# Kernel tuning notes

Measured on AMD Instinct MI355X. Metric: run time of the kernel, lower is better.

## Reference

```python
import jax, jax.numpy as jnp
import numpy as np

EMB = 2048
HEADS = 8
HEAD_DIM = EMB // HEADS  # 256

def setup_inputs() -> dict:
    key = jax.random.key(0)
    ks = jax.random.split(key, 4)
    b, n = 2, 2048
    x = jax.random.normal(ks[0], (b, n, EMB), dtype=jnp.float32)
    # Linear weights stored as [in, out] (y = x @ W + b)
    w_qkv = jax.random.normal(ks[1], (EMB, 3 * EMB), dtype=jnp.float32) * (EMB ** -0.5)
    b_qkv = jnp.zeros((3 * EMB,), dtype=jnp.float32)
    w_proj = jax.random.normal(ks[2], (EMB, EMB), dtype=jnp.float32) * (EMB ** -0.5)
    b_proj = jnp.zeros((EMB,), dtype=jnp.float32)
    return {"x": x, "w_qkv": w_qkv, "b_qkv": b_qkv, "w_proj": w_proj, "b_proj": b_proj}

def reference(x, w_qkv, b_qkv, w_proj, b_proj):
    b, n, _ = x.shape
    qkv = x @ w_qkv + b_qkv                                   # [b, n, 3*emb]
    # rearrange 'b n (h d qkv) -> qkv b h n d': qkv index is innermost
    qkv = qkv.reshape(b, n, HEADS, HEAD_DIM, 3)
    qkv = jnp.transpose(qkv, (4, 0, 2, 1, 3))                 # [3, b, h, n, d]
    q, k, v = qkv[0], qkv[1], qkv[2]
    energy = jnp.einsum('bhqd,bhkd->bhqk', q, k)              # [b, h, n, n]
    scaling = EMB ** 0.5
    # NOTE: faithful to source — softmax on UNSCALED logits, divide after.
    att = jax.nn.softmax(energy, axis=-1) / scaling
    out = jnp.einsum('bhal,bhlv->bhav', att, v)               # [b, h, n, d]
    out = jnp.transpose(out, (0, 2, 1, 3)).reshape(b, n, EMB)  # b n (h d)
    return out @ w_proj + b_proj
```

## Files before the change

kernel.cpp:

```cpp
#include <hip/hip_runtime.h>
#include <cstdint>
#include <cstddef>


typedef __bf16 bf16x8 __attribute__((ext_vector_type(8)));
typedef __bf16 bf16x2 __attribute__((ext_vector_type(2)));
typedef float f32x4 __attribute__((ext_vector_type(4)));

#define SCALE_INV 0.022097086912079608f

#define GLDS16(gp, lp)                                                        \
  __builtin_amdgcn_global_load_lds(                                           \
      (const __attribute__((address_space(1))) void*)(gp),                    \
      (__attribute__((address_space(3))) void*)(lp), 16, 0, 0)

__device__ inline void split8(const float4 v0, const float4 v1, bf16x8& hi,
                              bf16x8& lo) {
  float a[8] = {v0.x, v0.y, v0.z, v0.w, v1.x, v1.y, v1.z, v1.w};
  bf16x8 h, l;
#pragma unroll
  for (int i = 0; i < 8; i++) {
    __bf16 hh = (__bf16)a[i];
    h[i] = hh;
    l[i] = (__bf16)(a[i] - (float)hh);
  }
  hi = h;
  lo = l;
}

__global__ __launch_bounds__(256) void transpose_cvt_k(
    const float* __restrict__ in, __bf16* __restrict__ out, int R, int C) {
  __shared__ float tile[32][33];
  const int tx = threadIdx.x & 31;
  const int ty = threadIdx.x >> 5;
  const int c0 = blockIdx.x * 32;
  const int r0 = blockIdx.y * 32;
#pragma unroll
  for (int i = 0; i < 32; i += 8)
    tile[ty + i][tx] = in[(size_t)(r0 + ty + i) * C + (c0 + tx)];
  __syncthreads();
#pragma unroll
  for (int i = 0; i < 32; i += 8)
    out[(size_t)(c0 + ty + i) * R + (r0 + tx)] = (__bf16)tile[tx][ty + i];
}

__global__ __launch_bounds__(256) void transpose_w_split_k(
    const float* __restrict__ in, __bf16* __restrict__ wh,
    __bf16* __restrict__ wl1, __bf16* __restrict__ wl2) {
  __shared__ float tile[64][65];
  const int tid = threadIdx.x;
  const int c0 = blockIdx.x * 64;
  const int r0 = blockIdx.y * 64;
  const int cx = tid & 15, ry = tid >> 4;
#pragma unroll
  for (int p = 0; p < 4; p++) {
    const float4 v =
        *(const float4*)&in[(size_t)(r0 + p * 16 + ry) * 6144 + c0 + cx * 4];
    tile[p * 16 + ry][cx * 4 + 0] = v.x;
    tile[p * 16 + ry][cx * 4 + 1] = v.y;
    tile[p * 16 + ry][cx * 4 + 2] = v.z;
    tile[p * 16 + ry][cx * 4 + 3] = v.w;
  }
  __syncthreads();
  const int r2 = tid & 31;
  const int cy = tid >> 5;
  __bf16* wlb = (c0 < 2048) ? wl1 + (size_t)c0 * 2048
                            : wl2 + (size_t)(c0 - 2048) * 2048;
#pragma unroll
  for (int p = 0; p < 8; p++) {
    const int cl = cy + p * 8;
    const float t0 = tile[2 * r2][cl];
    const float t1 = tile[2 * r2 + 1][cl];
    const __bf16 h0 = (__bf16)t0, h1 = (__bf16)t1;
    bf16x2 hv = {h0, h1};
    bf16x2 lv = {(__bf16)(t0 - (float)h0), (__bf16)(t1 - (float)h1)};
    *(bf16x2*)&wh[(size_t)(c0 + cl) * 2048 + r0 + 2 * r2] = hv;
    *(bf16x2*)&wlb[(size_t)cl * 2048 + r0 + 2 * r2] = lv;
  }
}

__global__ __launch_bounds__(256) void gemm_qkv_split_k(
    const float* __restrict__ X, const __bf16* __restrict__ Wh,
    const __bf16* __restrict__ Wl1, const __bf16* __restrict__ Wl2,
    const float* __restrict__ bias, __bf16* __restrict__ qh_,
    __bf16* __restrict__ ql_, __bf16* __restrict__ kh_,
    __bf16* __restrict__ kl_, __bf16* __restrict__ vT) {
  __shared__ __bf16 Ah[128 * 40], Al[128 * 40];
  __shared__ __attribute__((aligned(16))) __bf16 BhL[2 * 4096];
  __shared__ __attribute__((aligned(16))) __bf16 BlL[2 * 4096];
  const int tid = threadIdx.x, lane = tid & 63, wave = tid >> 6;
  const int l16 = lane & 15, quad = lane >> 4;
  const int wm = (wave >> 1) * 64, wn = (wave & 1) * 64;
  const int bid = blockIdx.y * 48 + blockIdx.x;
  const int nb2 = (bid & 7) * 192 + (bid >> 3);
  const int m0 = (nb2 / 48) * 128, n0 = (nb2 % 48) * 128;
  const int r0 = tid >> 2, kc0 = (tid & 3) * 8;

  f32x4 zero4 = {0.f, 0.f, 0.f, 0.f};
  f32x4 acc[4][4];
#pragma unroll
  for (int i = 0; i < 4; i++)
#pragma unroll
    for (int j = 0; j < 4; j++) acc[i][j] = zero4;

  const float* Arow0 = X + (size_t)(m0 + r0) * 2048 + kc0;
  const float* Arow1 = Arow0 + (size_t)64 * 2048;
  const __bf16* BhP = Wh + (size_t)n0 * 2048;
  const __bf16* BlP = (n0 < 2048) ? Wl1 + (size_t)n0 * 2048
                                  : Wl2 + (size_t)(n0 - 2048) * 2048;

  const int rowl = lane >> 2, gq = lane & 3;
  const int sg = gq ^ (rowl & 3);
  size_t bSrc[2];
  int bDst[2];
#pragma unroll
  for (int i = 0; i < 2; i++) {
    const int row = wave * 32 + i * 16 + rowl;
    bSrc[i] = (size_t)row * 2048 + sg * 8;
    bDst[i] = (wave * 32 + i * 16) * 32;
  }
  const int bro = (wn + l16) * 32 + ((quad ^ (l16 & 3)) << 3);

  GLDS16(BhP + bSrc[0], &BhL[bDst[0]]);
  GLDS16(BhP + bSrc[1], &BhL[bDst[1]]);
  GLDS16(BlP + bSrc[0], &BlL[bDst[0]]);
  GLDS16(BlP + bSrc[1], &BlL[bDst[1]]);
  float4 a00 = *(const float4*)(Arow0);
  float4 a01 = *(const float4*)(Arow0 + 4);
  float4 a10 = *(const float4*)(Arow1);
  float4 a11 = *(const float4*)(Arow1 + 4);
  bf16x8 ah0, al0, ah1, al1;
  split8(a00, a01, ah0, al0);
  split8(a10, a11, ah1, al1);
  *(bf16x8*)&Ah[r0 * 40 + kc0] = ah0;
  *(bf16x8*)&Al[r0 * 40 + kc0] = al0;
  *(bf16x8*)&Ah[(r0 + 64) * 40 + kc0] = ah1;
  *(bf16x8*)&Al[(r0 + 64) * 40 + kc0] = al1;

  for (int k0 = 0; k0 < 2048; k0 += 32) {
    const int cur = (k0 >> 5) & 1;
    const int cb = cur * 4096;
    __syncthreads();
    const int nxt = k0 + 32;
    if (nxt < 2048) {
      const int nb = (cur ^ 1) * 4096;
      GLDS16(BhP + bSrc[0] + nxt, &BhL[nb + bDst[0]]);
      GLDS16(BhP + bSrc[1] + nxt, &BhL[nb + bDst[1]]);
      GLDS16(BlP + bSrc[0] + nxt, &BlL[nb + bDst[0]]);
      GLDS16(BlP + bSrc[1] + nxt, &BlL[nb + bDst[1]]);
      a00 = *(const float4*)(Arow0 + nxt);
      a01 = *(const float4*)(Arow0 + nxt + 4);
      a10 = *(const float4*)(Arow1 + nxt);
      a11 = *(const float4*)(Arow1 + nxt + 4);
    }
    bf16x8 fah[4], fal[4], fbh[4], fbl[4];
#pragma unroll
    for (int i = 0; i < 4; i++) {
      fah[i] = *(const bf16x8*)&Ah[(wm + i * 16 + l16) * 40 + quad * 8];
      fal[i] = *(const bf16x8*)&Al[(wm + i * 16 + l16) * 40 + quad * 8];
    }
#pragma unroll
    for (int j = 0; j < 4; j++) {
      fbh[j] = *(const bf16x8*)&BhL[cb + bro + j * 512];
      fbl[j] = *(const bf16x8*)&BlL[cb + bro + j * 512];
    }
#pragma unroll
    for (int i = 0; i < 4; i++)
#pragma unroll
      for (int j = 0; j < 4; j++) {
        acc[i][j] = __builtin_amdgcn_mfma_f32_16x16x32_bf16(fah[i], fbh[j],
                                                            acc[i][j], 0, 0, 0);
        acc[i][j] = __builtin_amdgcn_mfma_f32_16x16x32_bf16(fah[i], fbl[j],
                                                            acc[i][j], 0, 0, 0);
        acc[i][j] = __builtin_amdgcn_mfma_f32_16x16x32_bf16(fal[i], fbh[j],
                                                            acc[i][j], 0, 0, 0);
      }
    if (nxt < 2048) {
      split8(a00, a01, ah0, al0);
      split8(a10, a11, ah1, al1);
      __syncthreads();
      *(bf16x8*)&Ah[r0 * 40 + kc0] = ah0;
      *(bf16x8*)&Al[r0 * 40 + kc0] = al0;
      *(bf16x8*)&Ah[(r0 + 64) * 40 + kc0] = ah1;
      *(bf16x8*)&Al[(r0 + 64) * 40 + kc0] = al1;
    }
  }

#pragma unroll
  for (int i = 0; i < 4; i++) {
#pragma unroll
    for (int j = 0; j < 4; j++) {
      const int col = n0 + wn + j * 16 + l16;
      const float bv = bias[col];
      const int h = col / 768;
      const int rr = col - h * 768;
      const int d = rr / 3;
      const int c = rr - d * 3;
#pragma unroll
      for (int r = 0; r < 4; r++) {
        const int row = m0 + wm + i * 16 + quad * 4 + r;
        const float v = acc[i][j][r] + bv;
        const int b = row >> 11;
        const int nn = row & 2047;
        const int bh = b * 8 + h;
        const size_t idx = ((size_t)bh * 2048 + nn) * 256 + d;
        if (c == 0) {
          __bf16 hi = (__bf16)v;
          qh_[idx] = hi;
          ql_[idx] = (__bf16)(v - (float)hi);
        } else if (c == 1) {
          __bf16 hi = (__bf16)v;
          kh_[idx] = hi;
          kl_[idx] = (__bf16)(v - (float)hi);
        } else {
          vT[((size_t)bh * 256 + d) * 2048 + nn] = (__bf16)v;
        }
      }
    }
  }
}

__global__ __launch_bounds__(256, 2) void attn_fwd_k(
    const __bf16* __restrict__ Qh,
    const __bf16* __restrict__ Ql,
    const __bf16* __restrict__ Kh,
    const __bf16* __restrict__ Kl,
    const __bf16* __restrict__ Vt,
    __bf16* __restrict__ out) {
  __shared__ __attribute__((aligned(16))) __bf16 KhL[64 * 256];
  __shared__ __attribute__((aligned(16))) __bf16 KlL[64 * 256];
  __shared__ __attribute__((aligned(16))) __bf16 Plds[4][16 * 72];

  const int qblk = blockIdx.x;
  const int bh = blockIdx.y;
  const int bb = bh >> 3, hh = bh & 7;
  const int tid = threadIdx.x, lane = tid & 63, wave = tid >> 6;
  const int l16 = lane & 15, quad = lane >> 4;

  const size_t hqk = (size_t)bh * 2048 * 256;
  const __bf16* qhp = Qh + hqk;
  const __bf16* qlp = Ql + hqk;
  const __bf16* khp = Kh + hqk;
  const __bf16* klp = Kl + hqk;
  const __bf16* vp = Vt + (size_t)bh * 256 * 2048;

  const int qrow = qblk * 64 + wave * 16;

  bf16x8 qhf[8], qlf[8];
#pragma unroll
  for (int t = 0; t < 8; t++) {
    const size_t off = (size_t)(qrow + l16) * 256 + t * 32 + quad * 8;
    qhf[t] = *(const bf16x8*)&qhp[off];
    qlf[t] = *(const bf16x8*)&qlp[off];
  }

  f32x4 zero4 = {0.f, 0.f, 0.f, 0.f};
  f32x4 o[16];
#pragma unroll
  for (int dt = 0; dt < 16; dt++) o[dt] = zero4;
  float mrow[4], lrow[4];
#pragma unroll
  for (int r = 0; r < 4; r++) {
    mrow[r] = -3.0e38f;
    lrow[r] = 0.f;
  }

  int koff[8];
#pragma unroll
  for (int i = 0; i < 8; i++) {
    const int r = wave * 16 + i * 2 + (lane >> 5);
    const int cb = ((lane & 31) << 4) ^ ((r & 7) << 4);
    koff[i] = r * 256 + (cb >> 1);
  }
  const int ldsb = wave * 4096;

#pragma unroll
  for (int i = 0; i < 8; i++) {
    GLDS16(khp + koff[i], &KhL[ldsb + i * 512]);
    GLDS16(klp + koff[i], &KlL[ldsb + i * 512]);
  }

  for (int kv0 = 0; kv0 < 2048; kv0 += 64) {
    __syncthreads();

    f32x4 s[4];
#pragma unroll
    for (int j = 0; j < 4; j++) s[j] = zero4;
    __builtin_amdgcn_s_setprio(1);
#pragma unroll
    for (int j = 0; j < 4; j++) {
      const int row = j * 16 + l16;
      const int swz = (row & 7) << 3;
      const int rb = row * 256;
#pragma unroll
      for (int t = 0; t < 8; t++) {
        const int off = rb + ((t * 32 + quad * 8) ^ swz);
        bf16x8 khf = *(const bf16x8*)&KhL[off];
        bf16x8 klf = *(const bf16x8*)&KlL[off];
        s[j] =
            __builtin_amdgcn_mfma_f32_16x16x32_bf16(qhf[t], khf, s[j], 0, 0, 0);
        s[j] =
            __builtin_amdgcn_mfma_f32_16x16x32_bf16(qhf[t], klf, s[j], 0, 0, 0);
        s[j] =
            __builtin_amdgcn_mfma_f32_16x16x32_bf16(qlf[t], khf, s[j], 0, 0, 0);
      }
    }
    __builtin_amdgcn_s_setprio(0);
    __syncthreads();

    if (kv0 + 64 < 2048) {
      const int kvn = (kv0 + 64) * 256;
#pragma unroll
      for (int i = 0; i < 8; i++) {
        GLDS16(khp + kvn + koff[i], &KhL[ldsb + i * 512]);
        GLDS16(klp + kvn + koff[i], &KlL[ldsb + i * 512]);
      }
    }

    float mnew[4], alpha[4], psum[4];
#pragma unroll
    for (int r = 0; r < 4; r++) {
      float mx = fmaxf(fmaxf(s[0][r], s[1][r]), fmaxf(s[2][r], s[3][r]));
#pragma unroll
      for (int off = 1; off < 16; off <<= 1)
        mx = fmaxf(mx, __shfl_xor(mx, off, 16));
      mnew[r] = fmaxf(mrow[r], mx);
      alpha[r] = __expf(mrow[r] - mnew[r]);
      psum[r] = 0.f;
    }
#pragma unroll
    for (int j = 0; j < 4; j++)
#pragma unroll
      for (int r = 0; r < 4; r++) {
        float p = __expf(s[j][r] - mnew[r]);
        s[j][r] = p;
        psum[r] += p;
      }
#pragma unroll
    for (int r = 0; r < 4; r++) {
#pragma unroll
      for (int off = 1; off < 16; off <<= 1)
        psum[r] += __shfl_xor(psum[r], off, 16);
      lrow[r] = lrow[r] * alpha[r] + psum[r];
      mrow[r] = mnew[r];
    }
#pragma unroll
    for (int dt = 0; dt < 16; dt++) {
      o[dt][0] *= alpha[0];
      o[dt][1] *= alpha[1];
      o[dt][2] *= alpha[2];
      o[dt][3] *= alpha[3];
    }
#pragma unroll
    for (int j = 0; j < 4; j++)
#pragma unroll
      for (int r = 0; r < 4; r++)
        Plds[wave][(quad * 4 + r) * 72 + j * 16 + l16] = (__bf16)s[j][r];
    bf16x8 pa0 = *(const bf16x8*)&Plds[wave][l16 * 72 + quad * 8];
    bf16x8 pa1 = *(const bf16x8*)&Plds[wave][l16 * 72 + 32 + quad * 8];

    __builtin_amdgcn_s_setprio(1);
#pragma unroll
    for (int dt = 0; dt < 16; dt++) {
      const __bf16* vr = vp + (size_t)(dt * 16 + l16) * 2048 + kv0 + quad * 8;
      bf16x8 vf0 = *(const bf16x8*)vr;
      bf16x8 vf1 = *(const bf16x8*)(vr + 32);
      o[dt] = __builtin_amdgcn_mfma_f32_16x16x32_bf16(pa0, vf0, o[dt], 0, 0, 0);
      o[dt] = __builtin_amdgcn_mfma_f32_16x16x32_bf16(pa1, vf1, o[dt], 0, 0, 0);
    }
    __builtin_amdgcn_s_setprio(0);
  }

#pragma unroll
  for (int r = 0; r < 4; r++) {
    const float inv = SCALE_INV / lrow[r];
    const int n = qrow + quad * 4 + r;
    const size_t base = ((size_t)bb * 2048 + n) * 2048 + hh * 256;
#pragma unroll
    for (int dt = 0; dt < 16; dt++)
      out[base + dt * 16 + l16] = (__bf16)(o[dt][r] * inv);
  }
}

__global__ __launch_bounds__(256) void gemm_bt_k(
    const __bf16* __restrict__ A, const __bf16* __restrict__ Bt,
    const float* __restrict__ bias, int M, int Ncols, int K,
    float* __restrict__ outF) {
  __shared__ __bf16 As[128 * 40];
  __shared__ __bf16 Bs[128 * 40];
  const int tid = threadIdx.x, lane = tid & 63, wave = tid >> 6;
  const int l16 = lane & 15, quad = lane >> 4;
  const int wm = (wave >> 1) * 64, wn = (wave & 1) * 64;
  const int m0 = blockIdx.y * 128, n0 = blockIdx.x * 128;
  const int r0 = tid >> 2, kc0 = (tid & 3) * 8;

  f32x4 zero4 = {0.f, 0.f, 0.f, 0.f};
  f32x4 acc[4][4];
#pragma unroll
  for (int i = 0; i < 4; i++)
#pragma unroll
    for (int j = 0; j < 4; j++) acc[i][j] = zero4;

  const __bf16* Aptr = A + (size_t)(m0 + r0) * K + kc0;
  const __bf16* Bptr = Bt + (size_t)(n0 + r0) * K + kc0;
  const size_t rowstep = (size_t)64 * K;

  for (int k0 = 0; k0 < K; k0 += 32) {
    uint4 a0 = *(const uint4*)(Aptr + k0);
    uint4 a1 = *(const uint4*)(Aptr + rowstep + k0);
    uint4 b0 = *(const uint4*)(Bptr + k0);
    uint4 b1 = *(const uint4*)(Bptr + rowstep + k0);
    __syncthreads();
    *(uint4*)&As[r0 * 40 + kc0] = a0;
    *(uint4*)&As[(r0 + 64) * 40 + kc0] = a1;
    *(uint4*)&Bs[r0 * 40 + kc0] = b0;
    *(uint4*)&Bs[(r0 + 64) * 40 + kc0] = b1;
    __syncthreads();
    bf16x8 af[4], bfv[4];
#pragma unroll
    for (int i = 0; i < 4; i++)
      af[i] = *(const bf16x8*)&As[(wm + i * 16 + l16) * 40 + quad * 8];
#pragma unroll
    for (int j = 0; j < 4; j++)
      bfv[j] = *(const bf16x8*)&Bs[(wn + j * 16 + l16) * 40 + quad * 8];
#pragma unroll
    for (int i = 0; i < 4; i++)
#pragma unroll
      for (int j = 0; j < 4; j++)
        acc[i][j] = __builtin_amdgcn_mfma_f32_16x16x32_bf16(af[i], bfv[j],
                                                            acc[i][j], 0, 0, 0);
  }

#pragma unroll
  for (int i = 0; i < 4; i++)
#pragma unroll
    for (int j = 0; j < 4; j++) {
      const int col = n0 + wn + j * 16 + l16;
      const float bv = bias[col];
#pragma unroll
      for (int r = 0; r < 4; r++) {
        const int row = m0 + wm + i * 16 + quad * 4 + r;
        outF[(size_t)row * Ncols + col] = acc[i][j][r] + bv;
      }
    }
}

extern "C" void kernel_launch(void* const* d_in, const int* in_sizes, int n_in,
                              void* d_out, int out_size, void* d_ws,
                              size_t ws_size, hipStream_t stream) {
  const float* x = (const float*)d_in[0];
  const float* w_qkv = (const float*)d_in[1];
  const float* b_qkv = (const float*)d_in[2];
  const float* w_proj = (const float*)d_in[3];
  const float* b_proj = (const float*)d_in[4];
  float* out = (float*)d_out;

  const size_t HSZ = (size_t)16 * 2048 * 256;
  __bf16* qh = (__bf16*)d_ws;
  __bf16* ql = qh + HSZ;
  __bf16* kh = ql + HSZ;
  __bf16* kl = kh + HSZ;
  __bf16* vT = kl + HSZ;
  __bf16* attn = vT + HSZ;
  __bf16* wprojT = qh;

  __bf16* wh = (__bf16*)out;
  __bf16* wl1 = wh + (size_t)6144 * 2048;
  __bf16* wl2 = attn;

  transpose_w_split_k<<<dim3(96, 32), 256, 0, stream>>>(w_qkv, wh, wl1, wl2);
  gemm_qkv_split_k<<<dim3(48, 32), 256, 0, stream>>>(x, wh, wl1, wl2, b_qkv,
                                                     qh, ql, kh, kl, vT);
  attn_fwd_k<<<dim3(32, 16), 256, 0, stream>>>(qh, ql, kh, kl, vT, attn);
  transpose_cvt_k<<<dim3(64, 64), 256, 0, stream>>>(w_proj, wprojT, 2048, 2048);
  gemm_bt_k<<<dim3(16, 32), 256, 0, stream>>>(attn, wprojT, b_proj, 4096, 2048,
                                              2048, out);
}
```

Baseline: 973.5 us.

## Double-buffer A tile in QKV GEMM, drop mid-loop barrier, use linear block mapping

```diff
diff --git a/kernel.cpp b/kernel.cpp
--- a/kernel.cpp
+++ b/kernel.cpp
@@ -85,15 +85,13 @@
     const float* __restrict__ bias, __bf16* __restrict__ qh_,
     __bf16* __restrict__ ql_, __bf16* __restrict__ kh_,
     __bf16* __restrict__ kl_, __bf16* __restrict__ vT) {
-  __shared__ __bf16 Ah[128 * 40], Al[128 * 40];
-  __shared__ __attribute__((aligned(16))) __bf16 BhL[2 * 4096];
-  __shared__ __attribute__((aligned(16))) __bf16 BlL[2 * 4096];
+  __shared__ __bf16 Ah[2][128 * 40], Al[2][128 * 40];
+  __shared__ __attribute__((aligned(16))) __bf16 BhL[2][4096];
+  __shared__ __attribute__((aligned(16))) __bf16 BlL[2][4096];
   const int tid = threadIdx.x, lane = tid & 63, wave = tid >> 6;
   const int l16 = lane & 15, quad = lane >> 4;
   const int wm = (wave >> 1) * 64, wn = (wave & 1) * 64;
-  const int bid = blockIdx.y * 48 + blockIdx.x;
-  const int nb2 = (bid & 7) * 192 + (bid >> 3);
-  const int m0 = (nb2 / 48) * 128, n0 = (nb2 % 48) * 128;
+  const int m0 = blockIdx.y * 128, n0 = blockIdx.x * 128;
   const int r0 = tid >> 2, kc0 = (tid & 3) * 8;
 
   f32x4 zero4 = {0.f, 0.f, 0.f, 0.f};
@@ -121,48 +119,46 @@
   }
   const int bro = (wn + l16) * 32 + ((quad ^ (l16 & 3)) << 3);
 
-  GLDS16(BhP + bSrc[0], &BhL[bDst[0]]);
-  GLDS16(BhP + bSrc[1], &BhL[bDst[1]]);
-  GLDS16(BlP + bSrc[0], &BlL[bDst[0]]);
-  GLDS16(BlP + bSrc[1], &BlL[bDst[1]]);
   float4 a00 = *(const float4*)(Arow0);
   float4 a01 = *(const float4*)(Arow0 + 4);
   float4 a10 = *(const float4*)(Arow1);
   float4 a11 = *(const float4*)(Arow1 + 4);
+  GLDS16(BhP + bSrc[0], &BhL[0][bDst[0]]);
+  GLDS16(BhP + bSrc[1], &BhL[0][bDst[1]]);
+  GLDS16(BlP + bSrc[0], &BlL[0][bDst[0]]);
+  GLDS16(BlP + bSrc[1], &BlL[0][bDst[1]]);
   bf16x8 ah0, al0, ah1, al1;
   split8(a00, a01, ah0, al0);
   split8(a10, a11, ah1, al1);
-  *(bf16x8*)&Ah[r0 * 40 + kc0] = ah0;
-  *(bf16x8*)&Al[r0 * 40 + kc0] = al0;
-  *(bf16x8*)&Ah[(r0 + 64) * 40 + kc0] = ah1;
-  *(bf16x8*)&Al[(r0 + 64) * 40 + kc0] = al1;
+  *(bf16x8*)&Ah[0][r0 * 40 + kc0] = ah0;
+  *(bf16x8*)&Al[0][r0 * 40 + kc0] = al0;
+  *(bf16x8*)&Ah[0][(r0 + 64) * 40 + kc0] = ah1;
+  *(bf16x8*)&Al[0][(r0 + 64) * 40 + kc0] = al1;
 
   for (int k0 = 0; k0 < 2048; k0 += 32) {
     const int cur = (k0 >> 5) & 1;
-    const int cb = cur * 4096;
     __syncthreads();
     const int nxt = k0 + 32;
     if (nxt < 2048) {
-      const int nb = (cur ^ 1) * 4096;
-      GLDS16(BhP + bSrc[0] + nxt, &BhL[nb + bDst[0]]);
-      GLDS16(BhP + bSrc[1] + nxt, &BhL[nb + bDst[1]]);
-      GLDS16(BlP + bSrc[0] + nxt, &BlL[nb + bDst[0]]);
-      GLDS16(BlP + bSrc[1] + nxt, &BlL[nb + bDst[1]]);
       a00 = *(const float4*)(Arow0 + nxt);
       a01 = *(const float4*)(Arow0 + nxt + 4);
       a10 = *(const float4*)(Arow1 + nxt);
       a11 = *(const float4*)(Arow1 + nxt + 4);
+      GLDS16(BhP + bSrc[0] + nxt, &BhL[cur ^ 1][bDst[0]]);
+      GLDS16(BhP + bSrc[1] + nxt, &BhL[cur ^ 1][bDst[1]]);
+      GLDS16(BlP + bSrc[0] + nxt, &BlL[cur ^ 1][bDst[0]]);
+      GLDS16(BlP + bSrc[1] + nxt, &BlL[cur ^ 1][bDst[1]]);
     }
     bf16x8 fah[4], fal[4], fbh[4], fbl[4];
 #pragma unroll
     for (int i = 0; i < 4; i++) {
-      fah[i] = *(const bf16x8*)&Ah[(wm + i * 16 + l16) * 40 + quad * 8];
-      fal[i] = *(const bf16x8*)&Al[(wm + i * 16 + l16) * 40 + quad * 8];
+      fah[i] = *(const bf16x8*)&Ah[cur][(wm + i * 16 + l16) * 40 + quad * 8];
+      fal[i] = *(const bf16x8*)&Al[cur][(wm + i * 16 + l16) * 40 + quad * 8];
     }
 #pragma unroll
     for (int j = 0; j < 4; j++) {
-      fbh[j] = *(const bf16x8*)&BhL[cb + bro + j * 512];
-      fbl[j] = *(const bf16x8*)&BlL[cb + bro + j * 512];
+      fbh[j] = *(const bf16x8*)&BhL[cur][bro + j * 512];
+      fbl[j] = *(const bf16x8*)&BlL[cur][bro + j * 512];
     }
 #pragma unroll
     for (int i = 0; i < 4; i++)
@@ -178,11 +174,10 @@
     if (nxt < 2048) {
       split8(a00, a01, ah0, al0);
       split8(a10, a11, ah1, al1);
-      __syncthreads();
-      *(bf16x8*)&Ah[r0 * 40 + kc0] = ah0;
-      *(bf16x8*)&Al[r0 * 40 + kc0] = al0;
-      *(bf16x8*)&Ah[(r0 + 64) * 40 + kc0] = ah1;
-      *(bf16x8*)&Al[(r0 + 64) * 40 + kc0] = al1;
+      *(bf16x8*)&Ah[cur ^ 1][r0 * 40 + kc0] = ah0;
+      *(bf16x8*)&Al[cur ^ 1][r0 * 40 + kc0] = al0;
+      *(bf16x8*)&Ah[cur ^ 1][(r0 + 64) * 40 + kc0] = ah1;
+      *(bf16x8*)&Al[cur ^ 1][(r0 + 64) * 40 + kc0] = al1;
     }
   }
 
```

New measurement: 973.7 us. Within noise of the previous version (+0.0%).
